# Performance work log

Hardware: AMD Instinct MI355X
Metric: run time of the kernel (lower is better)

Reference implementation:

```python
import jax, jax.numpy as jnp
import numpy as np

B, N, R, D, K, T = 256, 2048, 64, 64, 2, 8  # graphs, nodes, roots, embed dim, in-degree, node types


def setup_inputs() -> dict:
    key = jax.random.key(0)
    k_root, k_w1, k_w2, k_types = jax.random.split(key, 4)
    rng = np.random.default_rng(0)
    # topologically valid DAG: parents of node i are drawn from [0, i)
    raw = rng.integers(0, 1 << 30, size=(B, N, K))
    denom = np.maximum(np.arange(N), 1)[None, :, None]
    node_inputs_indices = (raw % denom).astype(np.int32)
    node_types = jax.random.randint(k_types, (B, N), 0, T, dtype=jnp.int32)
    root_embeddings = jax.random.normal(k_root, (B, R, D), dtype=jnp.float32)
    # per-node-type encoder MLP: [K*D -> 2D -> D], GELU between layers
    W1 = jax.random.normal(k_w1, (T, K * D, 2 * D), dtype=jnp.float32) / np.sqrt(K * D)
    b1 = jnp.zeros((T, 2 * D), dtype=jnp.float32)
    W2 = jax.random.normal(k_w2, (T, 2 * D, D), dtype=jnp.float32) / np.sqrt(2 * D)
    b2 = jnp.zeros((T, D), dtype=jnp.float32)
    return {
        "root_embeddings": root_embeddings,
        "W1": W1,
        "b1": b1,
        "W2": W2,
        "b2": b2,
        "node_inputs_indices": jnp.asarray(node_inputs_indices),
        "node_types": node_types,
    }


def reference(root_embeddings, W1, b1, W2, b2, node_inputs_indices, node_types):
    buf0 = jnp.zeros((B, N, D), dtype=root_embeddings.dtype)
    buf0 = buf0.at[:, :R].set(root_embeddings)
    # per-step data for the sequential traversal over nodes R..N-1
    idx_seq = jnp.transpose(node_inputs_indices[:, R:, :], (1, 0, 2))  # [N-R, B, K]
    typ_seq = jnp.transpose(node_types[:, R:], (1, 0))                  # [N-R, B]
    pos_seq = jnp.arange(R, N)

    def step(buf, xs):
        idx, typ, pos = xs
        # gather parent embeddings: [B, K, D]
        parents = jnp.take_along_axis(buf, idx[:, :, None], axis=1)
        x = parents.reshape(B, K * D)
        h = jax.nn.gelu(jnp.einsum("bi,bih->bh", x, W1[typ]) + b1[typ], approximate=False)
        out = jnp.einsum("bh,bhd->bd", h, W2[typ]) + b2[typ]  # [B, D]
        buf = buf.at[:, pos].set(out)
        return buf, None

    buf, _ = jax.lax.scan(step, buf0, (idx_seq, typ_seq, pos_seq))
    return buf  # [B, N, D] full embeddings buffer
```

## Files before the change

kernel.cpp:

```cpp
#include <hip/hip_runtime.h>
#include <hip/hip_bf16.h>
#include <math.h>

#define NB 256
#define NN 2048
#define NR 64
#define ND 64
#define NT 8
#define NTH 512
#define NW 8
#define XP 136

typedef __attribute__((ext_vector_type(8))) short short8;
typedef __attribute__((ext_vector_type(4))) float f32x4;

__device__ __forceinline__ unsigned short f2bf(float f) {
    unsigned u = __float_as_uint(f);
    return (unsigned short)((u + 0x7fffu + ((u >> 16) & 1u)) >> 16);
}

__device__ __forceinline__ float fast_gelu(float v) {
    const float x  = v * 0.70710678118654752f;
    const float ax = fabsf(x);
    const float t  = __builtin_amdgcn_rcpf(fmaf(0.3275911f, ax, 1.0f));
    float p = fmaf(1.061405429f, t, -1.453152027f);
    p = fmaf(p, t, 1.421413741f);
    p = fmaf(p, t, -0.284496736f);
    p = fmaf(p, t, 0.254829592f);
    p *= t;
    const float e       = exp2f(ax * ax * -1.4426950408889634f);
    const float erf_abs = fmaf(-p, e, 1.0f);
    const float er      = copysignf(erf_abs, v);
    return 0.5f * v * (1.0f + er);
}

__global__ void convert_weights(const float* __restrict__ W1,
                                const float* __restrict__ W2,
                                unsigned short* __restrict__ w1t,
                                unsigned short* __restrict__ w2t) {
    int g = blockIdx.x * 256 + threadIdx.x;
    if (g < NT * 128 * 128) {
        int t = g >> 14, r = g & 16383, j = r >> 7, i = r & 127;
        w1t[g] = f2bf(W1[(t * 128 + i) * 128 + j]);
    }
    if (g < NT * 64 * 128) {
        int t = g >> 13, r = g & 8191, d = r >> 7, jj = r & 127;
        w2t[g] = f2bf(W2[(t * 128 + jj) * 64 + d]);
    }
}

__device__ __forceinline__ void block_scan2048(unsigned* __restrict__ arr,
                                               unsigned* __restrict__ csum,
                                               int w, int lane) {
    for (int c = w; c < 32; c += NW) {
        unsigned v = arr[c * 64 + lane];
        #pragma unroll
        for (int off = 1; off < 64; off <<= 1) {
            unsigned u = __shfl_up(v, off, 64);
            if (lane >= off) v += u;
        }
        arr[c * 64 + lane] = v;
        if (lane == 63) csum[c] = v;
    }
    __syncthreads();
    if (w == 0) {
        unsigned s = (lane < 32) ? csum[lane] : 0u;
        #pragma unroll
        for (int off = 1; off < 32; off <<= 1) {
            unsigned u = __shfl_up(s, off, 64);
            if (lane >= off) s += u;
        }
        if (lane < 32) csum[lane] = s;
    }
    __syncthreads();
    for (int c = w; c < 32; c += NW)
        if (c > 0) arr[c * 64 + lane] += csum[c - 1];
    __syncthreads();
}

__global__ __launch_bounds__(NTH, 2)
void dag_encoder_kernel(const float* __restrict__ roots,
                        const float* __restrict__ b1,
                        const float* __restrict__ b2,
                        const int*   __restrict__ idxs,
                        const int*   __restrict__ types,
                        float* __restrict__ out,
                        const unsigned short* __restrict__ w1t,
                        const unsigned short* __restrict__ w2t)
{
    __shared__ unsigned int   depth[NN];
    __shared__ unsigned short keys[NN];
    __shared__ unsigned int   scanA[NN];
    __shared__ unsigned short list[NN];
    __shared__ __align__(4) unsigned short parv[2 * NN];
    __shared__ unsigned int   csum[32];
    __shared__ __align__(16) unsigned short hs[NW][16][XP];
    __shared__ int s_maxd;

    const int b    = blockIdx.x;
    const int tid  = threadIdx.x;
    const int w    = tid >> 6;
    const int lane = tid & 63;
    const int q    = lane >> 4;
    const int l    = lane & 15;

    float* gbuf = out + (size_t)b * NN * ND;
    const int* gtyp = types + (size_t)b * NN;
    const int* gi   = idxs  + (size_t)b * NN * 2;

    {
        const float4* r4 = (const float4*)(roots + (size_t)b * NR * ND);
        float4* o4 = (float4*)gbuf;
        for (int i = tid; i < NR * ND / 4; i += NTH) o4[i] = r4[i];
        for (int i = tid; i < 2 * NN; i += NTH) parv[i] = (unsigned short)gi[i];
        for (int i = tid; i < NN; i += NTH) depth[i] = (i < NR) ? 0u : 0xFFFFFFFFu;
        for (int i = tid; i < NN; i += NTH) scanA[i] = 0;
        if (tid == 0) s_maxd = 0;
    }
    __syncthreads();

    if (w == 0) {
        for (int g0 = NR; g0 < NN; g0 += 64) {
            const int n  = g0 + lane;
            const int p0 = parv[2 * n];
            const int p1 = parv[2 * n + 1];
            bool done = false;
            #pragma unroll 1
            for (int iter = 0; iter < 64; ++iter) {
                if (!done) {
                    const unsigned d0 = depth[p0];
                    const unsigned d1 = depth[p1];
                    if (d0 != 0xFFFFFFFFu && d1 != 0xFFFFFFFFu) {
                        depth[n] = 1u + (d0 > d1 ? d0 : d1);
                        done = true;
                    }
                }
                if (__all(done)) break;
                asm volatile("s_waitcnt lgkmcnt(0)" ::: "memory");
            }
        }
    }
    __syncthreads();

    {
        unsigned mloc = 0;
        for (int i = tid; i < NN; i += NTH) {
            if (i >= NR) {
                unsigned lv = depth[i]; if (lv > 255u) lv = 255u;
                if (lv > mloc) mloc = lv;
                int key = (int)lv * 8 + gtyp[i];
                keys[i] = (unsigned short)key;
                atomicAdd(&scanA[key], 1u);
            }
        }
        atomicMax(&s_maxd, (int)mloc);
    }
    __syncthreads();

    block_scan2048(scanA, csum, w, lane);

    for (int i = tid; i < NN; i += NTH) depth[i] = (i == 0) ? 0u : scanA[i - 1];
    __syncthreads();

    for (int i = tid; i < NN; i += NTH) {
        if (i >= NR) {
            unsigned p = atomicAdd(&depth[keys[i]], 1u);
            list[p] = (unsigned short)i;
        }
    }
    __syncthreads();

    short8 w1f[32];
    #pragma unroll
    for (int n0 = 0; n0 < 8; ++n0)
        #pragma unroll
        for (int kk = 0; kk < 4; ++kk)
            w1f[n0 * 4 + kk] = *(const short8*)(w1t +
                ((size_t)(w * 128 + n0 * 16 + l) * 128 + kk * 32 + q * 8));
    short8 w2f[16];
    #pragma unroll
    for (int n0 = 0; n0 < 4; ++n0)
        #pragma unroll
        for (int kk = 0; kk < 4; ++kk)
            w2f[n0 * 4 + kk] = *(const short8*)(w2t +
                ((size_t)(w * 64 + n0 * 16 + l) * 128 + kk * 32 + q * 8));

    const int maxd = s_maxd;
    for (int L = 1; L <= maxd; ++L) {
        const int key = L * 8 + w;
        const unsigned seg = scanA[key - 1];
        const int cnt = (int)(scanA[key] - seg);
        for (int r0 = 0; r0 < cnt; r0 += 16) {
            const int rows = min(16, cnt - r0);

            const int rr   = min(l, rows - 1);
            const int node = list[seg + r0 + rr];
            const unsigned pcat = ((const unsigned*)parv)[node];
            const int p0 = (int)(pcat & 0xFFFFu), p1 = (int)(pcat >> 16);

            float4 ga[8];
            #pragma unroll
            for (int kk = 0; kk < 4; ++kk) {
                const float* s = gbuf + (size_t)(kk < 2 ? p0 : p1) * 64 + (kk & 1) * 32 + q * 8;
                ga[2 * kk]     = *(const float4*)s;
                ga[2 * kk + 1] = *(const float4*)(s + 4);
            }
            short8 af[4];
            #pragma unroll
            for (int kk = 0; kk < 4; ++kk) {
                short8 v;
                v[0] = (short)f2bf(ga[2 * kk].x);
                v[1] = (short)f2bf(ga[2 * kk].y);
                v[2] = (short)f2bf(ga[2 * kk].z);
                v[3] = (short)f2bf(ga[2 * kk].w);
                v[4] = (short)f2bf(ga[2 * kk + 1].x);
                v[5] = (short)f2bf(ga[2 * kk + 1].y);
                v[6] = (short)f2bf(ga[2 * kk + 1].z);
                v[7] = (short)f2bf(ga[2 * kk + 1].w);
                af[kk] = v;
            }

            #pragma unroll
            for (int h = 0; h < 2; ++h) {
                f32x4 c1[4];
                #pragma unroll
                for (int n0 = 0; n0 < 4; ++n0) c1[n0] = (f32x4){0.f, 0.f, 0.f, 0.f};
                #pragma unroll
                for (int kk = 0; kk < 4; ++kk)
                    #pragma unroll
                    for (int n0 = 0; n0 < 4; ++n0)
                        c1[n0] = __builtin_amdgcn_mfma_f32_16x16x32_bf16(
                            af[kk], w1f[(h * 4 + n0) * 4 + kk], c1[n0], 0, 0, 0);

                #pragma unroll
                for (int n0 = 0; n0 < 4; ++n0) {
                    const float bv = b1[w * 128 + (h * 4 + n0) * 16 + l];
                    #pragma unroll
                    for (int rg = 0; rg < 4; ++rg) {
                        const float v = c1[n0][rg] + bv;
                        hs[w][q * 4 + rg][(h * 4 + n0) * 16 + l] = f2bf(fast_gelu(v));
                    }
                }
            }
            asm volatile("s_waitcnt lgkmcnt(0)" ::: "memory");

            short8 a2[4];
            #pragma unroll
            for (int kk = 0; kk < 4; ++kk)
                a2[kk] = *(const short8*)&hs[w][l][kk * 32 + q * 8];
            f32x4 c2[4];
            #pragma unroll
            for (int n0 = 0; n0 < 4; ++n0) c2[n0] = (f32x4){0.f, 0.f, 0.f, 0.f};
            #pragma unroll
            for (int kk = 0; kk < 4; ++kk)
                #pragma unroll
                for (int n0 = 0; n0 < 4; ++n0)
                    c2[n0] = __builtin_amdgcn_mfma_f32_16x16x32_bf16(
                        a2[kk], w2f[n0 * 4 + kk], c2[n0], 0, 0, 0);

            #pragma unroll
            for (int n0 = 0; n0 < 4; ++n0) {
                const float bv2 = b2[w * 64 + n0 * 16 + l];
                #pragma unroll
                for (int rg = 0; rg < 4; ++rg) {
                    const int row = q * 4 + rg;
                    if (row < rows) {
                        const int nd = list[seg + r0 + row];
                        gbuf[nd * 64 + n0 * 16 + l] = c2[n0][rg] + bv2;
                    }
                }
            }
        }
        __syncthreads();
    }
}

extern "C" void kernel_launch(void* const* d_in, const int* in_sizes, int n_in,
                              void* d_out, int out_size, void* d_ws, size_t ws_size,
                              hipStream_t stream) {
    const float* roots = (const float*)d_in[0];
    const float* W1    = (const float*)d_in[1];
    const float* b1    = (const float*)d_in[2];
    const float* W2    = (const float*)d_in[3];
    const float* b2    = (const float*)d_in[4];
    const int*   idxs  = (const int*)d_in[5];
    const int*   types = (const int*)d_in[6];
    float*       outp  = (float*)d_out;

    unsigned short* w1t = (unsigned short*)d_ws;
    unsigned short* w2t = w1t + NT * 128 * 128;

    convert_weights<<<dim3(512), dim3(256), 0, stream>>>(W1, W2, w1t, w2t);
    dag_encoder_kernel<<<dim3(NB), dim3(NTH), 0, stream>>>(
        roots, b1, b2, idxs, types, outp, w1t, w2t);
}
```

Baseline: 378.1 us.

## Keep a bf16 mirror of embeddings in workspace for parent gathers

Adds a bf16 copy of the embedding buffer in workspace memory, written alongside each fp32 output. Parent gathers then read half as many bytes and skip the per-element fp32-to-bf16 conversion. It also precomputes parent index pairs per list slot, which removes one dependent shared-memory lookup. In exchange it adds extra global stores and needs enough workspace; if the workspace is too small the kernel falls back to the old path.

Result: slower. 418.8 us (+10.7%).

```diff
diff --git a/kernel.cpp b/kernel.cpp
--- a/kernel.cpp
+++ b/kernel.cpp
@@ -86,12 +86,14 @@
                         const int*   __restrict__ types,
                         float* __restrict__ out,
                         const unsigned short* __restrict__ w1t,
-                        const unsigned short* __restrict__ w2t)
+                        const unsigned short* __restrict__ w2t,
+                        unsigned short* __restrict__ mir)
 {
     __shared__ unsigned int   depth[NN];
     __shared__ unsigned short keys[NN];
     __shared__ unsigned int   scanA[NN];
     __shared__ unsigned short list[NN];
+    __shared__ unsigned int   listP[NN];
     __shared__ __align__(4) unsigned short parv[2 * NN];
     __shared__ unsigned int   csum[32];
     __shared__ __align__(16) unsigned short hs[NW][16][XP];
@@ -105,13 +107,22 @@
     const int l    = lane & 15;
 
     float* gbuf = out + (size_t)b * NN * ND;
+    unsigned short* mirg = mir ? (mir + (size_t)b * NN * ND) : (unsigned short*)0;
     const int* gtyp = types + (size_t)b * NN;
     const int* gi   = idxs  + (size_t)b * NN * 2;
 
     {
         const float4* r4 = (const float4*)(roots + (size_t)b * NR * ND);
         float4* o4 = (float4*)gbuf;
-        for (int i = tid; i < NR * ND / 4; i += NTH) o4[i] = r4[i];
+        for (int i = tid; i < NR * ND / 4; i += NTH) {
+            const float4 v = r4[i];
+            o4[i] = v;
+            if (mirg) {
+                unsigned lo = (unsigned)f2bf(v.x) | ((unsigned)f2bf(v.y) << 16);
+                unsigned hi = (unsigned)f2bf(v.z) | ((unsigned)f2bf(v.w) << 16);
+                *(uint2*)&mirg[i * 4] = make_uint2(lo, hi);
+            }
+        }
         for (int i = tid; i < 2 * NN; i += NTH) parv[i] = (unsigned short)gi[i];
         for (int i = tid; i < NN; i += NTH) depth[i] = (i < NR) ? 0u : 0xFFFFFFFFu;
         for (int i = tid; i < NN; i += NTH) scanA[i] = 0;
@@ -165,7 +176,8 @@
     for (int i = tid; i < NN; i += NTH) {
         if (i >= NR) {
             unsigned p = atomicAdd(&depth[keys[i]], 1u);
-            list[p] = (unsigned short)i;
+            list[p]  = (unsigned short)i;
+            listP[p] = ((const unsigned*)parv)[i];
         }
     }
     __syncthreads();
@@ -193,31 +205,39 @@
         for (int r0 = 0; r0 < cnt; r0 += 16) {
             const int rows = min(16, cnt - r0);
 
-            const int rr   = min(l, rows - 1);
-            const int node = list[seg + r0 + rr];
-            const unsigned pcat = ((const unsigned*)parv)[node];
+            const int rr = min(l, rows - 1);
+            const unsigned pcat = listP[seg + r0 + rr];
             const int p0 = (int)(pcat & 0xFFFFu), p1 = (int)(pcat >> 16);
 
-            float4 ga[8];
-            #pragma unroll
-            for (int kk = 0; kk < 4; ++kk) {
-                const float* s = gbuf + (size_t)(kk < 2 ? p0 : p1) * 64 + (kk & 1) * 32 + q * 8;
-                ga[2 * kk]     = *(const float4*)s;
-                ga[2 * kk + 1] = *(const float4*)(s + 4);
-            }
             short8 af[4];
-            #pragma unroll
-            for (int kk = 0; kk < 4; ++kk) {
-                short8 v;
-                v[0] = (short)f2bf(ga[2 * kk].x);
-                v[1] = (short)f2bf(ga[2 * kk].y);
-                v[2] = (short)f2bf(ga[2 * kk].z);
-                v[3] = (short)f2bf(ga[2 * kk].w);
-                v[4] = (short)f2bf(ga[2 * kk + 1].x);
-                v[5] = (short)f2bf(ga[2 * kk + 1].y);
-                v[6] = (short)f2bf(ga[2 * kk + 1].z);
-                v[7] = (short)f2bf(ga[2 * kk + 1].w);
-                af[kk] = v;
+            if (mirg) {
+                const unsigned short* m0 = mirg + (size_t)p0 * 64 + q * 8;
+                const unsigned short* m1 = mirg + (size_t)p1 * 64 + q * 8;
+                af[0] = *(const short8*)(m0);
+                af[1] = *(const short8*)(m0 + 32);
+                af[2] = *(const short8*)(m1);
+                af[3] = *(const short8*)(m1 + 32);
+            } else {
+                float4 ga[8];
+                #pragma unroll
+                for (int kk = 0; kk < 4; ++kk) {
+                    const float* s = gbuf + (size_t)(kk < 2 ? p0 : p1) * 64 + (kk & 1) * 32 + q * 8;
+                    ga[2 * kk]     = *(const float4*)s;
+                    ga[2 * kk + 1] = *(const float4*)(s + 4);
+                }
+                #pragma unroll
+                for (int kk = 0; kk < 4; ++kk) {
+                    short8 v;
+                    v[0] = (short)f2bf(ga[2 * kk].x);
+                    v[1] = (short)f2bf(ga[2 * kk].y);
+                    v[2] = (short)f2bf(ga[2 * kk].z);
+                    v[3] = (short)f2bf(ga[2 * kk].w);
+                    v[4] = (short)f2bf(ga[2 * kk + 1].x);
+                    v[5] = (short)f2bf(ga[2 * kk + 1].y);
+                    v[6] = (short)f2bf(ga[2 * kk + 1].z);
+                    v[7] = (short)f2bf(ga[2 * kk + 1].w);
+                    af[kk] = v;
+                }
             }
 
             #pragma unroll
@@ -266,7 +286,9 @@
                     const int row = q * 4 + rg;
                     if (row < rows) {
                         const int nd = list[seg + r0 + row];
-                        gbuf[nd * 64 + n0 * 16 + l] = c2[n0][rg] + bv2;
+                        const float val = c2[n0][rg] + bv2;
+                        gbuf[nd * 64 + n0 * 16 + l] = val;
+                        if (mirg) mirg[nd * 64 + n0 * 16 + l] = f2bf(val);
                     }
                 }
             }
@@ -289,8 +311,12 @@
 
     unsigned short* w1t = (unsigned short*)d_ws;
     unsigned short* w2t = w1t + NT * 128 * 128;
+    const size_t wbytes = (size_t)(NT * 128 * 128 + NT * 64 * 128) * 2;
+    const size_t mbytes = (size_t)NB * NN * ND * 2;
+    unsigned short* mirp = (ws_size >= wbytes + mbytes)
+        ? (unsigned short*)((char*)d_ws + wbytes) : (unsigned short*)0;
 
     convert_weights<<<dim3(512), dim3(256), 0, stream>>>(W1, W2, w1t, w2t);
     dag_encoder_kernel<<<dim3(NB), dim3(NTH), 0, stream>>>(
-        roots, b1, b2, idxs, types, outp, w1t, w2t);
-}
+        roots, b1, b2, idxs, types, outp, w1t, w2t, mirp);
+}
```
